# Performance work log

Measured on AMD Instinct MI355X. Metric: run time of the kernel, lower is better.

Reference implementation:

```python
import jax, jax.numpy as jnp
import numpy as np

N_NODES = 100000
N_EDGES = 1600000
IN_CH, EDGE_DIM, HIDDEN, OUT_CH = 3, 3, 64, 1


def setup_inputs() -> dict:
    key = jax.random.key(0)
    ks = jax.random.split(key, 10)
    x = jax.random.normal(ks[0], (N_NODES, IN_CH), dtype=jnp.float32)
    edge_index = jax.random.randint(ks[1], (2, N_EDGES), 0, N_NODES, dtype=jnp.int64)
    edge_attr = jax.random.normal(ks[2], (N_EDGES, EDGE_DIM), dtype=jnp.float32)
    # Linear params (torch Linear: y = x @ W.T + b); we store W as (in, out)
    s1 = 1.0 / np.sqrt(IN_CH + EDGE_DIM)
    W1 = jax.random.uniform(ks[3], (IN_CH + EDGE_DIM, HIDDEN), jnp.float32, -s1, s1)
    b1 = jax.random.uniform(ks[4], (HIDDEN,), jnp.float32, -s1, s1)
    s2 = 1.0 / np.sqrt(HIDDEN + EDGE_DIM)
    W2 = jax.random.uniform(ks[5], (HIDDEN + EDGE_DIM, HIDDEN), jnp.float32, -s2, s2)
    b2 = jax.random.uniform(ks[6], (HIDDEN,), jnp.float32, -s2, s2)
    s3 = 1.0 / np.sqrt(HIDDEN)
    W3 = jax.random.uniform(ks[7], (HIDDEN, OUT_CH), jnp.float32, -s3, s3)
    b3 = jax.random.uniform(ks[8], (OUT_CH,), jnp.float32, -s3, s3)
    return {"x": x, "edge_index": edge_index, "edge_attr": edge_attr,
            "W1": W1, "b1": b1, "W2": W2, "b2": b2, "W3": W3, "b3": b3}


def _edge_conv(h, src, dst, edge_attr, W, b, n_nodes):
    # gather source node features, concat edge_attr, linear, scatter-add at dst
    msg = jnp.concatenate([h[src], edge_attr], axis=-1) @ W + b  # [E, out]
    return jax.ops.segment_sum(msg, dst, num_segments=n_nodes)   # [N, out]


def reference(x, edge_index, edge_attr, W1, b1, W2, b2, W3, b3):
    src, dst = edge_index[0], edge_index[1]  # PyG source_to_target: aggregate at edge_index[1]
    n = x.shape[0]
    h = jax.nn.relu(_edge_conv(x, src, dst, edge_attr, W1, b1, n))
    h = jax.nn.relu(_edge_conv(h, src, dst, edge_attr, W2, b2, n))
    return h @ W3 + b3  # (n_nodes, 1) anomaly logits
```

## Files before the change

kernel.cpp:

```cpp
#include <hip/hip_runtime.h>

#define N_NODES 100000
#define N_EDGES 1600000
#define NCHUNK 256
#define CHUNK_E (N_EDGES / NCHUNK)
#define BSHIFT 6
#define BMASK 63
#define NBUCK 1563
#define REC_CAP 1536


typedef unsigned int uint4_ev __attribute__((ext_vector_type(4)));
typedef short bf16x8 __attribute__((ext_vector_type(8)));
typedef float f32x4 __attribute__((ext_vector_type(4)));

__device__ __forceinline__ unsigned short f2bf(float f) {
    unsigned int u = __float_as_uint(f);
    unsigned int r = (u + 0x7fff + ((u >> 16) & 1)) >> 16;
    return (unsigned short)r;
}
__device__ __forceinline__ unsigned int pack2bf(float a, float b) {
    return (unsigned int)f2bf(a) | ((unsigned int)f2bf(b) << 16);
}
__device__ __forceinline__ float bflo(unsigned int v) { return __uint_as_float(v << 16); }
__device__ __forceinline__ float bfhi(unsigned int v) { return __uint_as_float(v & 0xffff0000u); }

__device__ __forceinline__ float4 nt_load4(const float4* p) {
    uint4_ev v = __builtin_nontemporal_load((const uint4_ev*)p);
    return make_float4(__uint_as_float(v.x), __uint_as_float(v.y),
                       __uint_as_float(v.z), __uint_as_float(v.w));
}

__device__ __forceinline__ int wave_incl_scan(int v, int lane) {
#pragma unroll
    for (int off = 1; off < 64; off <<= 1) {
        int t = __shfl_up(v, off, 64);
        if (lane >= off) v += t;
    }
    return v;
}

__global__ __launch_bounds__(1024) void k_hist(const int* __restrict__ ei,
                                               int* __restrict__ tbl,
                                               const float* __restrict__ W2,
                                               unsigned short* __restrict__ wpk) {
    if (blockIdx.x == NCHUNK) {
        int i = threadIdx.x;
        if (i < 512) {
            int lane = i & 63, hh = (i >> 6) & 1, nt = i >> 7;
            int col = nt * 16 + (lane & 15);
            int k0 = hh * 32 + (lane >> 4) * 8;
#pragma unroll
            for (int j = 0; j < 8; j++)
                wpk[i * 8 + j] = f2bf(W2[(k0 + j) * 64 + col]);
        }
        return;
    }
    __shared__ int h[NBUCK];
    for (int i = threadIdx.x; i < NBUCK; i += 1024) h[i] = 0;
    __syncthreads();
    const int base = blockIdx.x * CHUNK_E;
    for (int i = threadIdx.x; i < CHUNK_E; i += 1024)
        atomicAdd(&h[ei[N_EDGES + base + i] >> BSHIFT], 1);
    __syncthreads();
    for (int i = threadIdx.x; i < NBUCK; i += 1024)
        tbl[blockIdx.x * NBUCK + i] = h[i];
}

__global__ __launch_bounds__(256) void k_colscan(int* __restrict__ tbl,
                                                 int* __restrict__ bsum) {
    const int b = blockIdx.x, t = threadIdx.x;
    int v = tbl[t * NBUCK + b];
    int lane = t & 63, w = t >> 6;
    int inc = wave_incl_scan(v, lane);
    __shared__ int ws[4];
    if (lane == 63) ws[w] = inc;
    __syncthreads();
    int wo = 0;
    for (int k = 0; k < w; k++) wo += ws[k];
    tbl[t * NBUCK + b] = wo + inc - v;
    if (t == 255) bsum[b] = wo + inc;
}

__global__ __launch_bounds__(1024) void k_basescan(const int* __restrict__ bsum,
                                                   int* __restrict__ bbase) {
    int t = threadIdx.x, lane = t & 63, w = t >> 6;
    int i0 = 2 * t, i1 = 2 * t + 1;
    int v0 = (i0 < NBUCK) ? bsum[i0] : 0;
    int v1 = (i1 < NBUCK) ? bsum[i1] : 0;
    int s = v0 + v1;
    int inc = wave_incl_scan(s, lane);
    __shared__ int ws[16];
    if (lane == 63) ws[w] = inc;
    __syncthreads();
    int wo = 0;
    for (int k = 0; k < w; k++) wo += ws[k];
    int excl = wo + inc - s;
    if (i0 < NBUCK) bbase[i0] = excl;
    if (i1 < NBUCK) bbase[i1] = excl + v0;
    if (i0 == NBUCK - 1) bbase[NBUCK] = excl + v0;
}

__global__ __launch_bounds__(1024) void k_scatter(const int* __restrict__ ei,
                                                  const float* __restrict__ ea,
                                                  const int* __restrict__ tbl,
                                                  const int* __restrict__ bbase,
                                                  float4* __restrict__ stg) {
    __shared__ int cur[NBUCK];
    for (int i = threadIdx.x; i < NBUCK; i += 1024)
        cur[i] = tbl[blockIdx.x * NBUCK + i] + bbase[i];
    __syncthreads();
    const int base = blockIdx.x * CHUNK_E;
    for (int i = threadIdx.x; i < CHUNK_E; i += 1024) {
        int e = base + i;
        int src = ei[e];
        int dst = ei[N_EDGES + e];
        float a0 = ea[(size_t)e * 3 + 0];
        float a1 = ea[(size_t)e * 3 + 1];
        float a2 = ea[(size_t)e * 3 + 2];
        int p = atomicAdd(&cur[dst >> BSHIFT], 1);
        unsigned pk = (unsigned)src | ((unsigned)(dst & BMASK) << 17);
        stg[p] = make_float4(__uint_as_float(pk), a0, a1, a2);
    }
}

__global__ __launch_bounds__(256) void k_finalize(
    const float4* __restrict__ stg, const int* __restrict__ bbase,
    const float* __restrict__ x, const float* __restrict__ W1,
    const float* __restrict__ b1, const float* __restrict__ W2,
    const float* __restrict__ b2, const bf16x8* __restrict__ wpk,
    int* __restrict__ csr, int* __restrict__ degp, int* __restrict__ rowend,
    unsigned int* __restrict__ zu, unsigned int* __restrict__ eu) {
    __shared__ float4 rec[REC_CAP];
    __shared__ int hist[64], lofs[64], cur[64];
    __shared__ float sU[64 * 3], sT[64 * 3];
    const int b = blockIdx.x, t = threadIdx.x;
    const int base = bbase[b], cnt = bbase[b + 1] - base;
    if (t < 64) hist[t] = 0;
    __syncthreads();
    const float* stgf = (const float*)stg;
    for (int i = t; i < cnt; i += 256) {
        unsigned pk = __float_as_uint(stgf[(size_t)(base + i) * 4]);
        atomicAdd(&hist[pk >> 17], 1);
    }
    __syncthreads();
    if (t < 64) {
        int v = hist[t];
        int inc = wave_incl_scan(v, t);
        lofs[t] = inc - v;
        cur[t] = inc - v;
    }
    __syncthreads();
    for (int i = t; i < cnt; i += 256) {
        float4 r = nt_load4(&stg[base + i]);
        unsigned pk = __float_as_uint(r.x);
        int p = atomicAdd(&cur[pk >> 17], 1);
        if (p < REC_CAP) rec[p] = r;
    }
    __syncthreads();
    {
        const int l = t >> 2, sub = t & 3;
        const int n = b * 64 + l;
        const int d = hist[l], lo = lofs[l];
        float u0 = 0, u1 = 0, u2 = 0, t0 = 0, t1 = 0, t2 = 0;
        for (int j = sub; j < d; j += 4) {
            float4 r = rec[lo + j];
            unsigned pk = __float_as_uint(r.x);
            int src = pk & 0x1FFFF;
            csr[base + lo + j] = src;
            t0 += r.y; t1 += r.z; t2 += r.w;
            u0 += x[src * 3 + 0]; u1 += x[src * 3 + 1]; u2 += x[src * 3 + 2];
        }
#pragma unroll
        for (int off = 1; off <= 2; off <<= 1) {
            u0 += __shfl_xor(u0, off, 64); u1 += __shfl_xor(u1, off, 64);
            u2 += __shfl_xor(u2, off, 64); t0 += __shfl_xor(t0, off, 64);
            t1 += __shfl_xor(t1, off, 64); t2 += __shfl_xor(t2, off, 64);
        }
        if (sub == 0) {
            sU[l * 3 + 0] = u0; sU[l * 3 + 1] = u1; sU[l * 3 + 2] = u2;
            sT[l * 3 + 0] = t0; sT[l * 3 + 1] = t1; sT[l * 3 + 2] = t2;
            if (n < N_NODES) {
                degp[n] = d;
                rowend[n] = base + lo + d;
            }
        }
    }
    __syncthreads();
    const int lane = t & 63, w = t >> 6;
    const int tb = b * 64 + w * 16;
    if (tb >= N_NODES) return;
    const int col = lane & 15;
    const int q = lane >> 4;
    const int ln = w * 16 + col;
    const float d = (float)hist[ln];
    const float u0 = sU[ln * 3], u1 = sU[ln * 3 + 1], u2 = sU[ln * 3 + 2];
    const float t0 = sT[ln * 3], t1 = sT[ln * 3 + 1], t2 = sT[ln * 3 + 2];
    bf16x8 af[2];
#pragma unroll
    for (int h = 0; h < 2; h++) {
#pragma unroll
        for (int j = 0; j < 8; j++) {
            int c = h * 32 + q * 8 + j;
            float a = d * b1[c];
            a = fmaf(u0, W1[0 * 64 + c], a);
            a = fmaf(u1, W1[1 * 64 + c], a);
            a = fmaf(u2, W1[2 * 64 + c], a);
            a = fmaf(t0, W1[3 * 64 + c], a);
            a = fmaf(t1, W1[4 * 64 + c], a);
            a = fmaf(t2, W1[5 * 64 + c], a);
            af[h][j] = (short)f2bf(fmaxf(a, 0.f));
        }
    }
    f32x4 acc[4];
#pragma unroll
    for (int nt = 0; nt < 4; nt++) {
        bf16x8 b0 = wpk[(nt * 2 + 0) * 64 + lane];
        bf16x8 b1f = wpk[(nt * 2 + 1) * 64 + lane];
        f32x4 a = {0.f, 0.f, 0.f, 0.f};
        a = __builtin_amdgcn_mfma_f32_16x16x32_bf16(af[0], b0, a, 0, 0, 0);
        a = __builtin_amdgcn_mfma_f32_16x16x32_bf16(af[1], b1f, a, 0, 0, 0);
        acc[nt] = a;
    }
#pragma unroll
    for (int nt = 0; nt < 4; nt++) {
#pragma unroll
        for (int r = 0; r < 4; r++) {
            float v = acc[nt][r];
            float pv = __shfl_xor(v, 1, 64);
            if ((lane & 1) == 0) {
                int nr = tb + q * 4 + r;
                zu[(size_t)nr * 32 + nt * 8 + (col >> 1)] = pack2bf(v, pv);
            }
        }
    }
    const float eb = b2[lane];
    const float w64 = W2[64 * 64 + lane];
    const float w65 = W2[65 * 64 + lane];
    const float w66 = W2[66 * 64 + lane];
#pragma unroll 4
    for (int mm = 0; mm < 16; mm++) {
        int lm = w * 16 + mm;
        float dd = (float)hist[lm];
        float s0 = sT[lm * 3], s1 = sT[lm * 3 + 1], s2 = sT[lm * 3 + 2];
        float e = dd * eb;
        e = fmaf(s0, w64, e); e = fmaf(s1, w65, e); e = fmaf(s2, w66, e);
        float pe = __shfl_xor(e, 1, 64);
        if ((lane & 1) == 0)
            eu[(size_t)(tb + mm) * 32 + (lane >> 1)] = pack2bf(e, pe);
    }
}

__global__ __launch_bounds__(256) void k_agg(
    const unsigned int* __restrict__ zu, const unsigned int* __restrict__ eu,
    const int* __restrict__ rowend, const int* __restrict__ degp,
    const int* __restrict__ csr, const float* __restrict__ W3,
    const float* __restrict__ b3, float* __restrict__ out) {
    const int lane = threadIdx.x & 63;
    const int li = lane & 15;
    const int q = li & 7;
    const int r = li >> 3;
    const int n = blockIdx.x * 16 + (threadIdx.x >> 4);

    float cw3[8];
#pragma unroll
    for (int m = 0; m < 8; m++) cw3[m] = W3[8 * q + m];
    const float b3v = b3[0];

    const int end = rowend[n], d = degp[n], start = end - d;
    float S[8];
#pragma unroll
    for (int m = 0; m < 8; m++) S[m] = 0.f;

    for (int c = start; c < end; c += 16) {
        int idx[8];
        float mk[8];
        uint4 v[8];
#pragma unroll
        for (int u = 0; u < 8; u++) {
            int i = c + 2 * u + r;
            bool ok = i < end;
            mk[u] = ok ? 1.f : 0.f;
            idx[u] = csr[ok ? i : start];
        }
#pragma unroll
        for (int u = 0; u < 8; u++)
            v[u] = *(const uint4*)&zu[(size_t)idx[u] * 32 + q * 4];
#pragma unroll
        for (int u = 0; u < 8; u++) {
            S[0] = fmaf(mk[u], bflo(v[u].x), S[0]); S[1] = fmaf(mk[u], bfhi(v[u].x), S[1]);
            S[2] = fmaf(mk[u], bflo(v[u].y), S[2]); S[3] = fmaf(mk[u], bfhi(v[u].y), S[3]);
            S[4] = fmaf(mk[u], bflo(v[u].z), S[4]); S[5] = fmaf(mk[u], bfhi(v[u].z), S[5]);
            S[6] = fmaf(mk[u], bflo(v[u].w), S[6]); S[7] = fmaf(mk[u], bfhi(v[u].w), S[7]);
        }
    }
#pragma unroll
    for (int m = 0; m < 8; m++) S[m] += __shfl_xor(S[m], 8, 64);

    const uint4 ev = *(const uint4*)&eu[(size_t)n * 32 + q * 4];
    float contrib;
    {
        float h0 = fmaxf(S[0] + bflo(ev.x), 0.f);
        float h1v = fmaxf(S[1] + bfhi(ev.x), 0.f);
        float h2v = fmaxf(S[2] + bflo(ev.y), 0.f);
        float h3 = fmaxf(S[3] + bfhi(ev.y), 0.f);
        float h4 = fmaxf(S[4] + bflo(ev.z), 0.f);
        float h5 = fmaxf(S[5] + bfhi(ev.z), 0.f);
        float h6 = fmaxf(S[6] + bflo(ev.w), 0.f);
        float h7 = fmaxf(S[7] + bfhi(ev.w), 0.f);
        contrib = h0 * cw3[0];
        contrib = fmaf(h1v, cw3[1], contrib);
        contrib = fmaf(h2v, cw3[2], contrib);
        contrib = fmaf(h3, cw3[3], contrib);
        contrib = fmaf(h4, cw3[4], contrib);
        contrib = fmaf(h5, cw3[5], contrib);
        contrib = fmaf(h6, cw3[6], contrib);
        contrib = fmaf(h7, cw3[7], contrib);
    }
    contrib += __shfl_xor(contrib, 1, 64);
    contrib += __shfl_xor(contrib, 2, 64);
    contrib += __shfl_xor(contrib, 4, 64);
    if (li == 0) out[n] = contrib + b3v;
}

extern "C" void kernel_launch(void* const* d_in, const int* in_sizes, int n_in,
                              void* d_out, int out_size, void* d_ws, size_t ws_size,
                              hipStream_t stream) {
    const float* x  = (const float*)d_in[0];
    const int*   ei = (const int*)d_in[1];
    const float* ea = (const float*)d_in[2];
    const float* W1 = (const float*)d_in[3];
    const float* b1 = (const float*)d_in[4];
    const float* W2 = (const float*)d_in[5];
    const float* b2 = (const float*)d_in[6];
    const float* W3 = (const float*)d_in[7];
    const float* b3 = (const float*)d_in[8];
    float* out = (float*)d_out;

    char* ws = (char*)d_ws;
    int*    tbl    = (int*)(ws + 0);
    int*    bsum   = (int*)(ws + 1600512);
    int*    bbase  = (int*)(ws + 1606912);
    int*    degp   = (int*)(ws + 1613312);
    int*    rowend = (int*)(ws + 2013440);
    int*    csr    = (int*)(ws + 2413568);
    float4* stg    = (float4*)(ws + 8813568);
    unsigned int* zu = (unsigned int*)(ws + 34413568);
    unsigned int* eu = (unsigned int*)(ws + 47213568);
    unsigned short* wpk = (unsigned short*)(ws + 60013568);

    k_hist<<<NCHUNK + 1, 1024, 0, stream>>>(ei, tbl, W2, wpk);
    k_colscan<<<NBUCK, 256, 0, stream>>>(tbl, bsum);
    k_basescan<<<1, 1024, 0, stream>>>(bsum, bbase);
    k_scatter<<<NCHUNK, 1024, 0, stream>>>(ei, ea, tbl, bbase, stg);
    k_finalize<<<NBUCK, 256, 0, stream>>>(stg, bbase, x, W1, b1, W2, b2,
                                          (const bf16x8*)wpk, csr, degp, rowend, zu, eu);
    k_agg<<<N_NODES / 16, 256, 0, stream>>>(zu, eu, rowend, degp, csr, W3, b3, out);
}
```

Baseline: 182.4 us.

## Replace bucket prefix-scan with fixed-capacity buckets and global atomic counters

```diff
diff --git a/kernel.cpp b/kernel.cpp
--- a/kernel.cpp
+++ b/kernel.cpp
@@ -7,6 +7,7 @@
 #define BSHIFT 6
 #define BMASK 63
 #define NBUCK 1563
+#define BCAP 1536
 #define REC_CAP 1536
 
 
@@ -40,10 +41,10 @@
     return v;
 }
 
-__global__ __launch_bounds__(1024) void k_hist(const int* __restrict__ ei,
-                                               int* __restrict__ tbl,
-                                               const float* __restrict__ W2,
-                                               unsigned short* __restrict__ wpk) {
+__global__ __launch_bounds__(1024) void k_scatter(
+    const int* __restrict__ ei, const float* __restrict__ ea,
+    int* __restrict__ bcnt, float4* __restrict__ stg,
+    const float* __restrict__ W2, unsigned short* __restrict__ wpk) {
     if (blockIdx.x == NCHUNK) {
         int i = threadIdx.x;
         if (i < 512) {
@@ -56,61 +57,18 @@
         }
         return;
     }
-    __shared__ int h[NBUCK];
+    __shared__ int h[NBUCK], cur[NBUCK];
     for (int i = threadIdx.x; i < NBUCK; i += 1024) h[i] = 0;
     __syncthreads();
     const int base = blockIdx.x * CHUNK_E;
     for (int i = threadIdx.x; i < CHUNK_E; i += 1024)
         atomicAdd(&h[ei[N_EDGES + base + i] >> BSHIFT], 1);
     __syncthreads();
-    for (int i = threadIdx.x; i < NBUCK; i += 1024)
-        tbl[blockIdx.x * NBUCK + i] = h[i];
-}
-
-__global__ __launch_bounds__(256) void k_colscan(int* __restrict__ tbl,
-                                                 int* __restrict__ bsum) {
-    const int b = blockIdx.x, t = threadIdx.x;
-    int v = tbl[t * NBUCK + b];
-    int lane = t & 63, w = t >> 6;
-    int inc = wave_incl_scan(v, lane);
-    __shared__ int ws[4];
-    if (lane == 63) ws[w] = inc;
-    __syncthreads();
-    int wo = 0;
-    for (int k = 0; k < w; k++) wo += ws[k];
-    tbl[t * NBUCK + b] = wo + inc - v;
-    if (t == 255) bsum[b] = wo + inc;
-}
-
-__global__ __launch_bounds__(1024) void k_basescan(const int* __restrict__ bsum,
-                                                   int* __restrict__ bbase) {
-    int t = threadIdx.x, lane = t & 63, w = t >> 6;
-    int i0 = 2 * t, i1 = 2 * t + 1;
-    int v0 = (i0 < NBUCK) ? bsum[i0] : 0;
-    int v1 = (i1 < NBUCK) ? bsum[i1] : 0;
-    int s = v0 + v1;
-    int inc = wave_incl_scan(s, lane);
-    __shared__ int ws[16];
-    if (lane == 63) ws[w] = inc;
-    __syncthreads();
-    int wo = 0;
-    for (int k = 0; k < w; k++) wo += ws[k];
-    int excl = wo + inc - s;
-    if (i0 < NBUCK) bbase[i0] = excl;
-    if (i1 < NBUCK) bbase[i1] = excl + v0;
-    if (i0 == NBUCK - 1) bbase[NBUCK] = excl + v0;
-}
-
-__global__ __launch_bounds__(1024) void k_scatter(const int* __restrict__ ei,
-                                                  const float* __restrict__ ea,
-                                                  const int* __restrict__ tbl,
-                                                  const int* __restrict__ bbase,
-                                                  float4* __restrict__ stg) {
-    __shared__ int cur[NBUCK];
-    for (int i = threadIdx.x; i < NBUCK; i += 1024)
-        cur[i] = tbl[blockIdx.x * NBUCK + i] + bbase[i];
-    __syncthreads();
-    const int base = blockIdx.x * CHUNK_E;
+    for (int i = threadIdx.x; i < NBUCK; i += 1024) {
+        int c = h[i];
+        if (c) cur[i] = i * BCAP + atomicAdd(&bcnt[i], c);
+    }
+    __syncthreads();
     for (int i = threadIdx.x; i < CHUNK_E; i += 1024) {
         int e = base + i;
         int src = ei[e];
@@ -125,7 +83,7 @@
 }
 
 __global__ __launch_bounds__(256) void k_finalize(
-    const float4* __restrict__ stg, const int* __restrict__ bbase,
+    const float4* __restrict__ stg, const int* __restrict__ bcnt,
     const float* __restrict__ x, const float* __restrict__ W1,
     const float* __restrict__ b1, const float* __restrict__ W2,
     const float* __restrict__ b2, const bf16x8* __restrict__ wpk,
@@ -135,7 +93,8 @@
     __shared__ int hist[64], lofs[64], cur[64];
     __shared__ float sU[64 * 3], sT[64 * 3];
     const int b = blockIdx.x, t = threadIdx.x;
-    const int base = bbase[b], cnt = bbase[b + 1] - base;
+    const int base = b * BCAP;
+    int cnt = bcnt[b]; if (cnt > BCAP) cnt = BCAP;
     if (t < 64) hist[t] = 0;
     __syncthreads();
     const float* stgf = (const float*)stg;
@@ -338,22 +297,18 @@
     float* out = (float*)d_out;
 
     char* ws = (char*)d_ws;
-    int*    tbl    = (int*)(ws + 0);
-    int*    bsum   = (int*)(ws + 1600512);
-    int*    bbase  = (int*)(ws + 1606912);
-    int*    degp   = (int*)(ws + 1613312);
-    int*    rowend = (int*)(ws + 2013440);
-    int*    csr    = (int*)(ws + 2413568);
-    float4* stg    = (float4*)(ws + 8813568);
-    unsigned int* zu = (unsigned int*)(ws + 34413568);
-    unsigned int* eu = (unsigned int*)(ws + 47213568);
-    unsigned short* wpk = (unsigned short*)(ws + 60013568);
-
-    k_hist<<<NCHUNK + 1, 1024, 0, stream>>>(ei, tbl, W2, wpk);
-    k_colscan<<<NBUCK, 256, 0, stream>>>(tbl, bsum);
-    k_basescan<<<1, 1024, 0, stream>>>(bsum, bbase);
-    k_scatter<<<NCHUNK, 1024, 0, stream>>>(ei, ea, tbl, bbase, stg);
-    k_finalize<<<NBUCK, 256, 0, stream>>>(stg, bbase, x, W1, b1, W2, b2,
+    int*    bcnt   = (int*)(ws + 0);
+    int*    degp   = (int*)(ws + 6400);
+    int*    rowend = (int*)(ws + 406400);
+    int*    csr    = (int*)(ws + 806400);
+    float4* stg    = (float4*)(ws + 10409600);
+    unsigned int* zu = (unsigned int*)(ws + 48821888);
+    unsigned int* eu = (unsigned int*)(ws + 61621888);
+    unsigned short* wpk = (unsigned short*)(ws + 74421888);
+
+    hipMemsetAsync(bcnt, 0, NBUCK * 4, stream);
+    k_scatter<<<NCHUNK + 1, 1024, 0, stream>>>(ei, ea, bcnt, stg, W2, wpk);
+    k_finalize<<<NBUCK, 256, 0, stream>>>(stg, bcnt, x, W1, b1, W2, b2,
                                           (const bf16x8*)wpk, csr, degp, rowend, zu, eu);
     k_agg<<<N_NODES / 16, 256, 0, stream>>>(zu, eu, rowend, degp, csr, W3, b3, out);
 }
```

Result: slower. 187.5 us (+2.8%).
